# Performance work log

Hardware: AMD Instinct MI355X
Metric: run time of the kernel (lower is better)

The kernel has to match this reference:

```python
import jax, jax.numpy as jnp
import numpy as np

B, T, C, H = 8, 2048, 1024, 64

def setup_inputs() -> dict:
    key = jax.random.key(0)
    k1, k2, k3, k4 = jax.random.split(key, 4)
    return {
        "inputs": jax.random.normal(k1, (B, T, C), dtype=jnp.float32),
        "Wq": jax.random.normal(k2, (C, H), dtype=jnp.float32) * (C ** -0.5),
        "Wk": jax.random.normal(k3, (C, H), dtype=jnp.float32) * (C ** -0.5),
        "Wv": jax.random.normal(k4, (C, H), dtype=jnp.float32) * (C ** -0.5),
    }

def reference(inputs, Wq, Wk, Wv):
    # q,k,v: [B,T,H]
    q = jnp.einsum('btc,ch->bth', inputs, Wq)
    k = jnp.einsum('btc,ch->bth', inputs, Wk)
    v = jnp.einsum('btc,ch->bth', inputs, Wv)
    c = inputs.shape[-1]
    # NOTE: original scales by C**-0.5 (embedding dim), not head_size**-0.5
    scale = jnp.asarray(c, inputs.dtype) ** -0.5
    wei = jnp.einsum('bqh,bkh->bqk', q, k) * scale  # [B,T,T]
    t = inputs.shape[1]
    causal = jnp.tril(jnp.ones((t, t), dtype=bool))
    wei = jnp.where(causal[None, :, :], wei, -jnp.inf)
    wei = jax.nn.softmax(wei, axis=-1)
    # dropout is identity in eval / DROP_RATE=0
    out = jnp.einsum('bqk,bkh->bqh', wei, v)  # [B,T,H]
    return out
```

## Files before the change

kernel.cpp:

```cpp
#include <hip/hip_runtime.h>
#include <stdint.h>

#define B_ 8
#define T_ 2048
#define C_ 1024
#define H_ 64
#define M_ (B_*T_)

typedef __bf16 bf16x8 __attribute__((ext_vector_type(8)));
typedef float  f32x4  __attribute__((ext_vector_type(4)));

union U4B { uint4 u; bf16x8 v; };

__device__ __forceinline__ unsigned short f32_to_bf16(float f) {
    union { float f; uint32_t u; } c; c.f = f;
    uint32_t u = c.u;
    u += 0x7fffu + ((u >> 16) & 1u);
    return (unsigned short)(u >> 16);
}
__device__ __forceinline__ uint32_t pack2_bf16(float a, float b) {
#if __has_builtin(__builtin_amdgcn_cvt_pk_bf16_f32)
    typedef __bf16 bf16x2 __attribute__((ext_vector_type(2)));
    union { bf16x2 v; uint32_t u; } c;
    c.v = __builtin_amdgcn_cvt_pk_bf16_f32(a, b);
    return c.u;
#else
    return (uint32_t)f32_to_bf16(a) | ((uint32_t)f32_to_bf16(b) << 16);
#endif
}

__global__ __launch_bounds__(256) void prepack_w(const float* __restrict__ Wq,
        const float* __restrict__ Wk, const float* __restrict__ Wv,
        unsigned short* __restrict__ wpk) {
    int o = blockIdx.x * 256 + threadIdx.x;
    if (o >= 24576) return;
    int lane = o & 63, nt = (o >> 6) % 12, kc = o / (64 * 12);
    int l15 = lane & 15, grp = lane >> 4;
    int n = nt * 16 + l15;
    int k = kc * 32 + grp * 8;
    const float* W = (n < 64) ? Wq : (n < 128) ? Wk : Wv;
    int col = n & 63;
    unsigned short tmp[8];
    #pragma unroll
    for (int j = 0; j < 8; j++) tmp[j] = f32_to_bf16(W[(size_t)(k + j) * 64 + col]);
    *(uint4*)(wpk + (size_t)o * 8) = *(uint4*)tmp;
}

__global__ __launch_bounds__(256) void convert_x(const float* __restrict__ X,
        unsigned short* __restrict__ xpk) {
    __shared__ unsigned short tl[16][144];
    const int t16 = blockIdx.x >> 3, kcg = blockIdx.x & 7;
    const int tid = threadIdx.x;
    const int wave = tid >> 6, lane = tid & 63;
    const int grp = lane >> 4, l15 = lane & 15;
    const int rr = tid >> 4, kk = (tid & 15) * 8;
    const float* xp = X + ((size_t)t16 * 16 + rr) * 1024 + kcg * 128 + kk;
    float4 f0 = *(const float4*)xp;
    float4 f1 = *(const float4*)(xp + 4);
    *(uint4*)&tl[rr][kk] = (uint4){ pack2_bf16(f0.x, f0.y), pack2_bf16(f0.z, f0.w),
                                    pack2_bf16(f1.x, f1.y), pack2_bf16(f1.z, f1.w) };
    __syncthreads();
    const int kc = kcg * 4 + wave;
    uint4 frag = *(const uint4*)&tl[l15][wave * 32 + grp * 8];
    *(uint4*)(xpk + ((size_t)(t16 * 32 + kc) * 64 + lane) * 8) = frag;
}

__global__ __launch_bounds__(256) void qkv_kernel(const unsigned short* __restrict__ xpk,
        const unsigned short* __restrict__ wpk,
        unsigned short* __restrict__ qb, unsigned short* __restrict__ kb,
        unsigned short* __restrict__ vt) {
    __shared__ unsigned short Wl[2][12][64][8];
    const int tid = threadIdx.x;
    const int wave = tid >> 6, lane = tid & 63;
    const int grp = lane >> 4, l15 = lane & 15;
    const int i = wave & 1, h = wave >> 1;
    const int t16 = blockIdx.x * 2 + i;

    f32x4 acc[6];
    #pragma unroll
    for (int j = 0; j < 6; j++) acc[j] = (f32x4){0.f, 0.f, 0.f, 0.f};

    const unsigned short* wsrc = wpk + (size_t)tid * 8;
    unsigned short* wdst0 = &Wl[0][0][0][0] + (size_t)tid * 8;
    unsigned short* wdst1 = &Wl[1][0][0][0] + (size_t)tid * 8;

    uint4 w0 = *(const uint4*)(wsrc);
    uint4 w1 = *(const uint4*)(wsrc + 256 * 8);
    uint4 w2 = *(const uint4*)(wsrc + 512 * 8);
    *(uint4*)(wdst0) = w0;
    *(uint4*)(wdst0 + 256 * 8) = w1;
    *(uint4*)(wdst0 + 512 * 8) = w2;
    U4B a_cur;
    a_cur.u = *(const uint4*)(xpk + ((size_t)(t16 * 32 + 0) * 64 + lane) * 8);
    __syncthreads();

    for (int kc = 0; kc < 32; kc++) {
        const int buf = kc & 1;
        U4B a_nxt;
        if (kc < 31) {
            const unsigned short* wn = wsrc + (size_t)(kc + 1) * 768 * 8;
            w0 = *(const uint4*)(wn);
            w1 = *(const uint4*)(wn + 256 * 8);
            w2 = *(const uint4*)(wn + 512 * 8);
            a_nxt.u = *(const uint4*)(xpk + ((size_t)(t16 * 32 + kc + 1) * 64 + lane) * 8);
        }
        #pragma unroll
        for (int jj = 0; jj < 6; jj++) {
            bf16x8 bfr = *(const bf16x8*)&Wl[buf][h * 6 + jj][lane][0];
            acc[jj] = __builtin_amdgcn_mfma_f32_16x16x32_bf16(a_cur.v, bfr, acc[jj], 0, 0, 0);
        }
        if (kc < 31) {
            unsigned short* wd = buf ? wdst0 : wdst1;
            *(uint4*)(wd) = w0;
            *(uint4*)(wd + 256 * 8) = w1;
            *(uint4*)(wd + 512 * 8) = w2;
            a_cur = a_nxt;
        }
        __syncthreads();
    }

    const int r0 = t16 * 16 + grp * 4;
    const int bb = r0 >> 11;
    const int t0 = r0 & 2047;
    #pragma unroll
    for (int jj = 0; jj < 6; jj++) {
        int col = (h * 6 + jj) * 16 + l15;
        if (col < 64) {
            for (int r = 0; r < 4; r++)
                qb[(size_t)(r0 + r) * 64 + col] = f32_to_bf16(acc[jj][r] * 0.03125f);
        } else if (col < 128) {
            for (int r = 0; r < 4; r++)
                kb[(size_t)(r0 + r) * 64 + (col - 64)] = f32_to_bf16(acc[jj][r]);
        } else {
            int c = col - 128;
            ushort4 vv;
            vv.x = f32_to_bf16(acc[jj][0]); vv.y = f32_to_bf16(acc[jj][1]);
            vv.z = f32_to_bf16(acc[jj][2]); vv.w = f32_to_bf16(acc[jj][3]);
            *(ushort4*)(vt + ((size_t)bb * 64 + c) * 2048 + t0) = vv;
        }
    }
}

__global__ __launch_bounds__(256) void attn1_kernel(const unsigned short* __restrict__ qb,
        const unsigned short* __restrict__ kb, const unsigned short* __restrict__ vt,
        float* __restrict__ pl, float* __restrict__ pacc) {
    __shared__ unsigned short Kl[64][72];
    __shared__ unsigned short Vl[64][72];
    const int tid = threadIdx.x;
    const int wave = tid >> 6, lane = tid & 63;
    const int grp = lane >> 4, l15 = lane & 15;
    const int b = blockIdx.x & 7;
    int f = blockIdx.x >> 3;
    int g = 0;
    for (; g < 32; g++) { int c = (35 - g) >> 2; if (f < c) break; f -= c; }
    const int j = 31 - g;
    const int s = f;
    const int ktend = min(4, (j + 1) - 4 * s);
    const int qbase = j * 64 + wave * 16;

    const unsigned short* qp = qb + ((size_t)b * 2048 + qbase + l15) * 64 + grp * 8;
    bf16x8 bq0 = *(const bf16x8*)qp;
    bf16x8 bq1 = *(const bf16x8*)(qp + 32);

    float lsum = 0.f;
    f32x4 acc[4];
    for (int d = 0; d < 4; d++) acc[d] = (f32x4){0.f, 0.f, 0.f, 0.f};

    const unsigned short* kB = kb + ((size_t)b * 2048 + s * 256) * 64;
    const unsigned short* vB = vt + (size_t)b * 64 * 2048 + s * 256;
    const int r1 = tid >> 3, c1 = (tid & 7) * 8;
    const int r2 = (tid + 256) >> 3, c2 = c1;

    uint4 kr0, kr1, vr0, vr1;
    kr0 = *(const uint4*)(kB + (size_t)r1 * 64 + c1);
    kr1 = *(const uint4*)(kB + (size_t)r2 * 64 + c2);
    vr0 = *(const uint4*)(vB + (size_t)r1 * 2048 + c1);
    vr1 = *(const uint4*)(vB + (size_t)r2 * 2048 + c2);

    for (int kt = 0; kt < ktend; kt++) {
        *(uint4*)&Kl[r1][c1] = kr0;  *(uint4*)&Kl[r2][c2] = kr1;
        *(uint4*)&Vl[r1][c1] = vr0;  *(uint4*)&Vl[r2][c2] = vr1;
        __syncthreads();
        if (kt + 1 < ktend) {
            const unsigned short* kN = kB + (size_t)(kt + 1) * 64 * 64;
            const unsigned short* vN = vB + (kt + 1) * 64;
            kr0 = *(const uint4*)(kN + (size_t)r1 * 64 + c1);
            kr1 = *(const uint4*)(kN + (size_t)r2 * 64 + c2);
            vr0 = *(const uint4*)(vN + (size_t)r1 * 2048 + c1);
            vr1 = *(const uint4*)(vN + (size_t)r2 * 2048 + c2);
        }
        const int keybase = s * 256 + kt * 64;
        f32x4 st[4];
        #pragma unroll
        for (int nt = 0; nt < 4; nt++) {
            bf16x8 a0 = *(const bf16x8*)&Kl[nt * 16 + l15][grp * 8];
            bf16x8 a1 = *(const bf16x8*)&Kl[nt * 16 + l15][32 + grp * 8];
            f32x4 t = (f32x4){0.f, 0.f, 0.f, 0.f};
            t = __builtin_amdgcn_mfma_f32_16x16x32_bf16(a0, bq0, t, 0, 0, 0);
            t = __builtin_amdgcn_mfma_f32_16x16x32_bf16(a1, bq1, t, 0, 0, 0);
            st[nt] = t;
        }
        if (keybase + 63 > qbase) {
            int q = qbase + l15;
            #pragma unroll
            for (int nt = 0; nt < 4; nt++)
                for (int r = 0; r < 4; r++)
                    if (keybase + nt * 16 + grp * 4 + r > q) st[nt][r] = -1e30f;
        }
        float p[4][4];
        #pragma unroll
        for (int nt = 0; nt < 4; nt++)
            for (int r = 0; r < 4; r++) { p[nt][r] = __expf(st[nt][r]); lsum += p[nt][r]; }
        uint32_t t0a = pack2_bf16(p[0][0], p[0][1]), t0b = pack2_bf16(p[0][2], p[0][3]);
        uint32_t t1a = pack2_bf16(p[1][0], p[1][1]), t1b = pack2_bf16(p[1][2], p[1][3]);
        uint32_t t2a = pack2_bf16(p[2][0], p[2][1]), t2b = pack2_bf16(p[2][2], p[2][3]);
        uint32_t t3a = pack2_bf16(p[3][0], p[3][1]), t3b = pack2_bf16(p[3][2], p[3][3]);
        const int s0l = ((grp & 1) << 5) + l15, s1l = s0l + 16;
        const bool hi = (grp >= 2);
        U4B bw0, bw1;
        {
            uint32_t e0a = (uint32_t)__shfl((int)t0a, s0l, 64);
            uint32_t e0b = (uint32_t)__shfl((int)t0b, s0l, 64);
            uint32_t e0c = (uint32_t)__shfl((int)t0a, s1l, 64);
            uint32_t e0d = (uint32_t)__shfl((int)t0b, s1l, 64);
            uint32_t e1a = (uint32_t)__shfl((int)t1a, s0l, 64);
            uint32_t e1b = (uint32_t)__shfl((int)t1b, s0l, 64);
            uint32_t e1c = (uint32_t)__shfl((int)t1a, s1l, 64);
            uint32_t e1d = (uint32_t)__shfl((int)t1b, s1l, 64);
            bw0.u = (uint4){ hi ? e1a : e0a, hi ? e1b : e0b, hi ? e1c : e0c, hi ? e1d : e0d };
        }
        {
            uint32_t e0a = (uint32_t)__shfl((int)t2a, s0l, 64);
            uint32_t e0b = (uint32_t)__shfl((int)t2b, s0l, 64);
            uint32_t e0c = (uint32_t)__shfl((int)t2a, s1l, 64);
            uint32_t e0d = (uint32_t)__shfl((int)t2b, s1l, 64);
            uint32_t e1a = (uint32_t)__shfl((int)t3a, s0l, 64);
            uint32_t e1b = (uint32_t)__shfl((int)t3b, s0l, 64);
            uint32_t e1c = (uint32_t)__shfl((int)t3a, s1l, 64);
            uint32_t e1d = (uint32_t)__shfl((int)t3b, s1l, 64);
            bw1.u = (uint4){ hi ? e1a : e0a, hi ? e1b : e0b, hi ? e1c : e0c, hi ? e1d : e0d };
        }
        #pragma unroll
        for (int dt = 0; dt < 4; dt++) {
            bf16x8 av0 = *(const bf16x8*)&Vl[dt * 16 + l15][grp * 8];
            bf16x8 av1 = *(const bf16x8*)&Vl[dt * 16 + l15][32 + grp * 8];
            acc[dt] = __builtin_amdgcn_mfma_f32_16x16x32_bf16(av0, bw0.v, acc[dt], 0, 0, 0);
            acc[dt] = __builtin_amdgcn_mfma_f32_16x16x32_bf16(av1, bw1.v, acc[dt], 0, 0, 0);
        }
        __syncthreads();
    }
    lsum += __shfl_xor(lsum, 16, 64);
    lsum += __shfl_xor(lsum, 32, 64);
    size_t rowq = (size_t)b * 2048 + qbase + l15;
    size_t p = rowq * 8 + s;
    if (grp == 0) pl[p] = lsum;
    #pragma unroll
    for (int dt = 0; dt < 4; dt++)
        *(f32x4*)&pacc[p * 64 + dt * 16 + grp * 4] = acc[dt];
}

__global__ __launch_bounds__(256) void attn2_kernel(const float* __restrict__ pl,
        const float* __restrict__ pacc, float* __restrict__ out) {
    int idx = blockIdx.x * 256 + threadIdx.x;
    int row = idx >> 4;
    int d0 = (idx & 15) * 4;
    int t = row & 2047;
    int ns = ((t >> 6) + 4) >> 2;
    float den = 0.f;
    f32x4 num = (f32x4){0.f, 0.f, 0.f, 0.f};
    for (int s = 0; s < ns; s++) {
        den += pl[(size_t)row * 8 + s];
        num += *(const f32x4*)&pacc[((size_t)row * 8 + s) * 64 + d0];
    }
    float inv = 1.f / den;
    *(f32x4*)&out[(size_t)row * 64 + d0] = num * inv;
}

extern "C" void kernel_launch(void* const* d_in, const int* in_sizes, int n_in,
                              void* d_out, int out_size, void* d_ws, size_t ws_size,
                              hipStream_t stream) {
    const float* X  = (const float*)d_in[0];
    const float* Wq = (const float*)d_in[1];
    const float* Wk = (const float*)d_in[2];
    const float* Wv = (const float*)d_in[3];
    float* out = (float*)d_out;

    unsigned short* qb  = (unsigned short*)d_ws;
    unsigned short* kb  = qb + (size_t)M_ * 64;
    unsigned short* wpk = kb + (size_t)M_ * 64;
    unsigned short* vt  = wpk + (size_t)24576 * 8;
    unsigned short* xpk = vt + (size_t)B_ * 64 * 2048;
    float* pl   = (float*)(xpk + (size_t)M_ * 1024);
    float* pacc = pl + (size_t)M_ * 8;

    prepack_w<<<96, 256, 0, stream>>>(Wq, Wk, Wv, wpk);
    convert_x<<<8192, 256, 0, stream>>>(X, xpk);
    qkv_kernel<<<512, 256, 0, stream>>>(xpk, wpk, qb, kb, vt);
    attn1_kernel<<<1152, 256, 0, stream>>>(qb, kb, vt, pl, pacc);
    attn2_kernel<<<1024, 256, 0, stream>>>(pl, pacc, out);
}
```

Baseline: 140.0 us.

## Merge weight and input prep kernels; widen attention key tile to 128

Folds the weight prepack and input conversion into one launch, with extra blocks handling the weights, which saves a kernel launch. The attention partial kernel now processes 128 keys per iteration instead of 64, halving barrier and loop overhead. It also drops the register prefetch double buffering in favour of load-then-store per iteration. For odd tile counts the second half reads keys beyond the valid range, which are masked to zero weight, but that is extra work and the loads may go out of bounds of the segment. Larger LDS use may also reduce occupancy.

```diff
diff --git a/kernel.cpp b/kernel.cpp
--- a/kernel.cpp
+++ b/kernel.cpp
@@ -29,26 +29,25 @@
 #endif
 }
 
-__global__ __launch_bounds__(256) void prepack_w(const float* __restrict__ Wq,
-        const float* __restrict__ Wk, const float* __restrict__ Wv,
+__global__ __launch_bounds__(256) void prep_kernel(const float* __restrict__ X,
+        const float* __restrict__ Wq, const float* __restrict__ Wk,
+        const float* __restrict__ Wv, unsigned short* __restrict__ xpk,
         unsigned short* __restrict__ wpk) {
-    int o = blockIdx.x * 256 + threadIdx.x;
-    if (o >= 24576) return;
-    int lane = o & 63, nt = (o >> 6) % 12, kc = o / (64 * 12);
-    int l15 = lane & 15, grp = lane >> 4;
-    int n = nt * 16 + l15;
-    int k = kc * 32 + grp * 8;
-    const float* W = (n < 64) ? Wq : (n < 128) ? Wk : Wv;
-    int col = n & 63;
-    unsigned short tmp[8];
-    #pragma unroll
-    for (int j = 0; j < 8; j++) tmp[j] = f32_to_bf16(W[(size_t)(k + j) * 64 + col]);
-    *(uint4*)(wpk + (size_t)o * 8) = *(uint4*)tmp;
-}
-
-__global__ __launch_bounds__(256) void convert_x(const float* __restrict__ X,
-        unsigned short* __restrict__ xpk) {
     __shared__ unsigned short tl[16][144];
+    if (blockIdx.x >= 8192) {
+        int o = (blockIdx.x - 8192) * 256 + threadIdx.x;
+        int lane = o & 63, nt = (o >> 6) % 12, kc = o / (64 * 12);
+        int l15 = lane & 15, grp = lane >> 4;
+        int n = nt * 16 + l15;
+        int k = kc * 32 + grp * 8;
+        const float* W = (n < 64) ? Wq : (n < 128) ? Wk : Wv;
+        int col = n & 63;
+        unsigned short tmp[8];
+        #pragma unroll
+        for (int j = 0; j < 8; j++) tmp[j] = f32_to_bf16(W[(size_t)(k + j) * 64 + col]);
+        *(uint4*)(wpk + (size_t)o * 8) = *(uint4*)tmp;
+        return;
+    }
     const int t16 = blockIdx.x >> 3, kcg = blockIdx.x & 7;
     const int tid = threadIdx.x;
     const int wave = tid >> 6, lane = tid & 63;
@@ -144,8 +143,8 @@
 __global__ __launch_bounds__(256) void attn1_kernel(const unsigned short* __restrict__ qb,
         const unsigned short* __restrict__ kb, const unsigned short* __restrict__ vt,
         float* __restrict__ pl, float* __restrict__ pacc) {
-    __shared__ unsigned short Kl[64][72];
-    __shared__ unsigned short Vl[64][72];
+    __shared__ unsigned short Kl[128][72];
+    __shared__ unsigned short Vl[64][136];
     const int tid = threadIdx.x;
     const int wave = tid >> 6, lane = tid & 63;
     const int grp = lane >> 4, l15 = lane & 15;
@@ -156,6 +155,7 @@
     const int j = 31 - g;
     const int s = f;
     const int ktend = min(4, (j + 1) - 4 * s);
+    const int nIter = (ktend + 1) >> 1;
     const int qbase = j * 64 + wave * 16;
 
     const unsigned short* qp = qb + ((size_t)b * 2048 + qbase + l15) * 64 + grp * 8;
@@ -168,31 +168,26 @@
 
     const unsigned short* kB = kb + ((size_t)b * 2048 + s * 256) * 64;
     const unsigned short* vB = vt + (size_t)b * 64 * 2048 + s * 256;
-    const int r1 = tid >> 3, c1 = (tid & 7) * 8;
-    const int r2 = (tid + 256) >> 3, c2 = c1;
-
-    uint4 kr0, kr1, vr0, vr1;
-    kr0 = *(const uint4*)(kB + (size_t)r1 * 64 + c1);
-    kr1 = *(const uint4*)(kB + (size_t)r2 * 64 + c2);
-    vr0 = *(const uint4*)(vB + (size_t)r1 * 2048 + c1);
-    vr1 = *(const uint4*)(vB + (size_t)r2 * 2048 + c2);
-
-    for (int kt = 0; kt < ktend; kt++) {
-        *(uint4*)&Kl[r1][c1] = kr0;  *(uint4*)&Kl[r2][c2] = kr1;
-        *(uint4*)&Vl[r1][c1] = vr0;  *(uint4*)&Vl[r2][c2] = vr1;
+    const int krow = tid >> 3, kcol = (tid & 7) * 8;
+    const int vrow = tid >> 4, vcol = (tid & 15) * 8;
+
+    for (int it = 0; it < nIter; it++) {
+        const int kt0 = it * 128;
+        uint4 kr[4], vr[4];
+        #pragma unroll
+        for (int i = 0; i < 4; i++) {
+            kr[i] = *(const uint4*)(kB + (size_t)(kt0 + krow + 32 * i) * 64 + kcol);
+            vr[i] = *(const uint4*)(vB + (size_t)(vrow + 16 * i) * 2048 + kt0 + vcol);
+        }
+        #pragma unroll
+        for (int i = 0; i < 4; i++) {
+            *(uint4*)&Kl[krow + 32 * i][kcol] = kr[i];
+            *(uint4*)&Vl[vrow + 16 * i][vcol] = vr[i];
+        }
         __syncthreads();
-        if (kt + 1 < ktend) {
-            const unsigned short* kN = kB + (size_t)(kt + 1) * 64 * 64;
-            const unsigned short* vN = vB + (kt + 1) * 64;
-            kr0 = *(const uint4*)(kN + (size_t)r1 * 64 + c1);
-            kr1 = *(const uint4*)(kN + (size_t)r2 * 64 + c2);
-            vr0 = *(const uint4*)(vN + (size_t)r1 * 2048 + c1);
-            vr1 = *(const uint4*)(vN + (size_t)r2 * 2048 + c2);
-        }
-        const int keybase = s * 256 + kt * 64;
-        f32x4 st[4];
-        #pragma unroll
-        for (int nt = 0; nt < 4; nt++) {
+        f32x4 st[8];
+        #pragma unroll
+        for (int nt = 0; nt < 8; nt++) {
             bf16x8 a0 = *(const bf16x8*)&Kl[nt * 16 + l15][grp * 8];
             bf16x8 a1 = *(const bf16x8*)&Kl[nt * 16 + l15][32 + grp * 8];
             f32x4 t = (f32x4){0.f, 0.f, 0.f, 0.f};
@@ -200,52 +195,44 @@
             t = __builtin_amdgcn_mfma_f32_16x16x32_bf16(a1, bq1, t, 0, 0, 0);
             st[nt] = t;
         }
-        if (keybase + 63 > qbase) {
+        const int keybase = s * 256 + kt0;
+        if (keybase + 127 > qbase) {
             int q = qbase + l15;
             #pragma unroll
-            for (int nt = 0; nt < 4; nt++)
+            for (int nt = 0; nt < 8; nt++)
                 for (int r = 0; r < 4; r++)
                     if (keybase + nt * 16 + grp * 4 + r > q) st[nt][r] = -1e30f;
         }
-        float p[4][4];
-        #pragma unroll
-        for (int nt = 0; nt < 4; nt++)
+        float p[8][4];
+        #pragma unroll
+        for (int nt = 0; nt < 8; nt++)
             for (int r = 0; r < 4; r++) { p[nt][r] = __expf(st[nt][r]); lsum += p[nt][r]; }
-        uint32_t t0a = pack2_bf16(p[0][0], p[0][1]), t0b = pack2_bf16(p[0][2], p[0][3]);
-        uint32_t t1a = pack2_bf16(p[1][0], p[1][1]), t1b = pack2_bf16(p[1][2], p[1][3]);
-        uint32_t t2a = pack2_bf16(p[2][0], p[2][1]), t2b = pack2_bf16(p[2][2], p[2][3]);
-        uint32_t t3a = pack2_bf16(p[3][0], p[3][1]), t3b = pack2_bf16(p[3][2], p[3][3]);
         const int s0l = ((grp & 1) << 5) + l15, s1l = s0l + 16;
         const bool hi = (grp >= 2);
-        U4B bw0, bw1;
-        {
-            uint32_t e0a = (uint32_t)__shfl((int)t0a, s0l, 64);
-            uint32_t e0b = (uint32_t)__shfl((int)t0b, s0l, 64);
-            uint32_t e0c = (uint32_t)__shfl((int)t0a, s1l, 64);
-            uint32_t e0d = (uint32_t)__shfl((int)t0b, s1l, 64);
-            uint32_t e1a = (uint32_t)__shfl((int)t1a, s0l, 64);
-            uint32_t e1b = (uint32_t)__shfl((int)t1b, s0l, 64);
-            uint32_t e1c = (uint32_t)__shfl((int)t1a, s1l, 64);
-            uint32_t e1d = (uint32_t)__shfl((int)t1b, s1l, 64);
-            bw0.u = (uint4){ hi ? e1a : e0a, hi ? e1b : e0b, hi ? e1c : e0c, hi ? e1d : e0d };
-        }
-        {
-            uint32_t e0a = (uint32_t)__shfl((int)t2a, s0l, 64);
-            uint32_t e0b = (uint32_t)__shfl((int)t2b, s0l, 64);
-            uint32_t e0c = (uint32_t)__shfl((int)t2a, s1l, 64);
-            uint32_t e0d = (uint32_t)__shfl((int)t2b, s1l, 64);
-            uint32_t e1a = (uint32_t)__shfl((int)t3a, s0l, 64);
-            uint32_t e1b = (uint32_t)__shfl((int)t3b, s0l, 64);
-            uint32_t e1c = (uint32_t)__shfl((int)t3a, s1l, 64);
-            uint32_t e1d = (uint32_t)__shfl((int)t3b, s1l, 64);
-            bw1.u = (uint4){ hi ? e1a : e0a, hi ? e1b : e0b, hi ? e1c : e0c, hi ? e1d : e0d };
+        U4B bw[4];
+        #pragma unroll
+        for (int half = 0; half < 4; half++) {
+            uint32_t ta0 = pack2_bf16(p[half * 2][0], p[half * 2][1]);
+            uint32_t tb0 = pack2_bf16(p[half * 2][2], p[half * 2][3]);
+            uint32_t ta1 = pack2_bf16(p[half * 2 + 1][0], p[half * 2 + 1][1]);
+            uint32_t tb1 = pack2_bf16(p[half * 2 + 1][2], p[half * 2 + 1][3]);
+            uint32_t e0a = (uint32_t)__shfl((int)ta0, s0l, 64);
+            uint32_t e0b = (uint32_t)__shfl((int)tb0, s0l, 64);
+            uint32_t e0c = (uint32_t)__shfl((int)ta0, s1l, 64);
+            uint32_t e0d = (uint32_t)__shfl((int)tb0, s1l, 64);
+            uint32_t e1a = (uint32_t)__shfl((int)ta1, s0l, 64);
+            uint32_t e1b = (uint32_t)__shfl((int)tb1, s0l, 64);
+            uint32_t e1c = (uint32_t)__shfl((int)ta1, s1l, 64);
+            uint32_t e1d = (uint32_t)__shfl((int)tb1, s1l, 64);
+            bw[half].u = (uint4){ hi ? e1a : e0a, hi ? e1b : e0b, hi ? e1c : e0c, hi ? e1d : e0d };
         }
         #pragma unroll
         for (int dt = 0; dt < 4; dt++) {
-            bf16x8 av0 = *(const bf16x8*)&Vl[dt * 16 + l15][grp * 8];
-            bf16x8 av1 = *(const bf16x8*)&Vl[dt * 16 + l15][32 + grp * 8];
-            acc[dt] = __builtin_amdgcn_mfma_f32_16x16x32_bf16(av0, bw0.v, acc[dt], 0, 0, 0);
-            acc[dt] = __builtin_amdgcn_mfma_f32_16x16x32_bf16(av1, bw1.v, acc[dt], 0, 0, 0);
+            #pragma unroll
+            for (int half = 0; half < 4; half++) {
+                bf16x8 av = *(const bf16x8*)&Vl[dt * 16 + l15][half * 32 + grp * 8];
+                acc[dt] = __builtin_amdgcn_mfma_f32_16x16x32_bf16(av, bw[half].v, acc[dt], 0, 0, 0);
+            }
         }
         __syncthreads();
     }
@@ -293,8 +280,7 @@
     float* pl   = (float*)(xpk + (size_t)M_ * 1024);
     float* pacc = pl + (size_t)M_ * 8;
 
-    prepack_w<<<96, 256, 0, stream>>>(Wq, Wk, Wv, wpk);
-    convert_x<<<8192, 256, 0, stream>>>(X, xpk);
+    prep_kernel<<<8288, 256, 0, stream>>>(X, Wq, Wk, Wv, xpk, wpk);
     qkv_kernel<<<512, 256, 0, stream>>>(xpk, wpk, qb, kb, vt);
     attn1_kernel<<<1152, 256, 0, stream>>>(qb, kb, vt, pl, pacc);
     attn2_kernel<<<1024, 256, 0, stream>>>(pl, pacc, out);
```

Result: slower. 142.9 us (+2.1%).
